# Kernel optimization log

Hardware: AMD Instinct MI355X
Metric: run time of the kernel (lower is better)

Reference implementation:

```python
import jax, jax.numpy as jnp
import numpy as np

B, N, D_IN, D_HID, D_OUT = 8, 512, 4608, 4608, 1152
DROP = 0.1
INV_SQRT2 = 0.7071067811865476
INV_SQRT_2PI = 0.3989422804014327


def _clean(s):
    # nan -> 1e-5, inf -> 1.0 (matches torch.where chain)
    return jnp.where(jnp.isnan(s), jnp.asarray(1e-5, s.dtype),
                     jnp.where(jnp.isinf(s), jnp.asarray(1.0, s.dtype), s))


def kl_regularizer(w_mu, w_sigma):
    d = w_mu.shape[0]
    ws = jax.nn.softplus(w_sigma)  # log(1+exp(w_sigma))
    return 0.5 * jnp.mean(d * ws + jnp.sum(w_mu * w_mu, axis=0) - d - d * jnp.log(ws))


def vdp_linear(mu_in, Sigma_in, w_mu, w_sigma):
    mu_out = jnp.matmul(mu_in, w_mu)                                 # [B,N,U]
    kl = kl_regularizer(w_mu, w_sigma)
    W_Sigma = jax.nn.softplus(w_sigma)                               # [U]
    Sigma_1 = jnp.matmul(Sigma_in, w_mu * w_mu)                      # w^T Sigma_in w (diag)
    Sigma_2 = jnp.sum(mu_in * mu_in, axis=-1, keepdims=True) * W_Sigma
    Sigma_3 = jnp.sum(Sigma_in, axis=-1, keepdims=True) * W_Sigma
    return mu_out, _clean(Sigma_1 + Sigma_2 + Sigma_3), kl


def vdp_gelu(mu_in, Sigma_in):
    # exact (erf) gelu and its analytic derivative: Phi(x) + x*phi(x)
    cdf = 0.5 * (1.0 + jax.lax.erf(mu_in * INV_SQRT2))
    pdf = jnp.exp(-0.5 * mu_in * mu_in) * INV_SQRT_2PI
    grad = cdf + mu_in * pdf
    return mu_in * cdf, grad * grad * Sigma_in


def vdp_dropout(mu_in, Sigma_in, mask):
    keep = 1.0 - DROP
    m = mask.astype(mu_in.dtype)
    mu_out = mu_in * m / keep                       # torch F.dropout scaling
    Sigma_out = Sigma_in * m / mu_in.shape[-1]      # kept Sigma values (unscaled), / units
    return mu_out, _clean(Sigma_out)


def setup_inputs() -> dict:
    key = jax.random.key(0)
    k = jax.random.split(key, 8)
    mu_in = jax.random.normal(k[0], (B, N, D_IN), dtype=jnp.float32)
    sigma_in = jax.random.uniform(k[1], (B, N, D_IN), dtype=jnp.float32)
    mask1 = jax.random.bernoulli(k[2], 1.0 - DROP, (B, N, D_HID))
    mask2 = jax.random.bernoulli(k[3], 1.0 - DROP, (B, N, D_OUT))
    w_mu1 = 0.05 * jax.random.normal(k[4], (D_IN, D_HID), dtype=jnp.float32)
    w_sigma1 = jnp.full((D_HID,), -4.6, dtype=jnp.float32)
    w_mu2 = 0.05 * jax.random.normal(k[5], (D_HID, D_OUT), dtype=jnp.float32)
    w_sigma2 = jnp.full((D_OUT,), -4.6, dtype=jnp.float32)
    return {"mu_in": mu_in, "sigma_in": sigma_in, "mask1": mask1, "mask2": mask2,
            "w_mu1": w_mu1, "w_sigma1": w_sigma1, "w_mu2": w_mu2, "w_sigma2": w_sigma2}


def reference(mu_in, sigma_in, mask1, mask2, w_mu1, w_sigma1, w_mu2, w_sigma2):
    mu, sig, kl1 = vdp_linear(mu_in, sigma_in, w_mu1, w_sigma1)
    mu, sig = vdp_gelu(mu, sig)
    mu, sig = vdp_dropout(mu, sig, mask1)
    mu, sig, kl2 = vdp_linear(mu, sig, w_mu2, w_sigma2)
    mu, sig = vdp_dropout(mu, sig, mask2)
    return mu, _clean(sig), kl1 + kl2
```

## Files before the change

kernel.cpp:

```cpp
#include <hip/hip_runtime.h>
#include <cstdint>
#include <cstddef>

static constexpr int Mrows = 4096;
static constexpr int K1 = 4608;
static constexpr int N1 = 4608;
static constexpr int N2 = 1152;
static constexpr int NPART1 = (K1 / 32) * (N1 / 32);
static constexpr int NPART2 = (K1 / 32) * (N2 / 32);

typedef float  f32x4  __attribute__((ext_vector_type(4)));
typedef __bf16 bf16x8 __attribute__((ext_vector_type(8)));

__device__ __forceinline__ unsigned short f2bf(float f) {
  unsigned int u = __float_as_uint(f);
  u += 0x7fffu + ((u >> 16) & 1u);
  return (unsigned short)(u >> 16);
}
__device__ __forceinline__ float bf2f(unsigned short h) {
  return __uint_as_float(((unsigned int)h) << 16);
}
__device__ __forceinline__ float cleanf(float s) {
  if (__builtin_isnan(s)) return 1e-5f;
  if (__builtin_isinf(s)) return 1.0f;
  return s;
}

__global__ __launch_bounds__(256) void prep_in(
    const float* __restrict__ mu, const float* __restrict__ sg,
    unsigned short* __restrict__ A1, unsigned short* __restrict__ As16,
    float* __restrict__ rmu2, float* __restrict__ rsg)
{
  const int row = blockIdx.x;
  const int tid = threadIdx.x;
  const float4* mup = (const float4*)(mu + (size_t)row * K1);
  const float4* sgp = (const float4*)(sg + (size_t)row * K1);
  ushort4* a1p = (ushort4*)(A1 + (size_t)row * K1);
  ushort4* asp = (ushort4*)(As16 + (size_t)row * K1);
  float smu = 0.f, ssg = 0.f;
  for (int j = tid; j < K1 / 4; j += 256) {
    float4 m4 = mup[j];
    float4 s4 = sgp[j];
    smu += m4.x*m4.x + m4.y*m4.y + m4.z*m4.z + m4.w*m4.w;
    ssg += s4.x + s4.y + s4.z + s4.w;
    a1p[j] = make_ushort4(f2bf(m4.x), f2bf(m4.y), f2bf(m4.z), f2bf(m4.w));
    asp[j] = make_ushort4(f2bf(s4.x), f2bf(s4.y), f2bf(s4.z), f2bf(s4.w));
  }
  __shared__ float red[2][4];
  for (int off = 32; off; off >>= 1) {
    smu += __shfl_down(smu, off);
    ssg += __shfl_down(ssg, off);
  }
  const int lane = tid & 63, wv = tid >> 6;
  if (!lane) { red[0][wv] = smu; red[1][wv] = ssg; }
  __syncthreads();
  if (tid == 0) {
    rmu2[row] = red[0][0] + red[0][1] + red[0][2] + red[0][3];
    rsg[row]  = red[1][0] + red[1][1] + red[1][2] + red[1][3];
  }
}

__global__ __launch_bounds__(256) void prep_w(
    const float* __restrict__ w, unsigned short* __restrict__ Bt,
    unsigned short* __restrict__ Bsq, float* __restrict__ partials,
    int K, int N)
{
  __shared__ float t[32][33];
  const int kt = blockIdx.x * 32;
  const int nt = blockIdx.y * 32;
  const int tx = threadIdx.x & 31;
  const int ty = threadIdx.x >> 5;
  float loc = 0.f;
#pragma unroll
  for (int i = 0; i < 32; i += 8) {
    float v = w[(size_t)(kt + ty + i) * N + (nt + tx)];
    t[ty + i][tx] = v;
    loc += v * v;
  }
  __syncthreads();
#pragma unroll
  for (int i = 0; i < 32; i += 8) {
    float v = t[tx][ty + i];
    size_t o = (size_t)(nt + ty + i) * K + (kt + tx);
    Bt[o]  = f2bf(v);
    Bsq[o] = f2bf(v * v);
  }
  __shared__ float red[4];
  for (int off = 32; off; off >>= 1) loc += __shfl_down(loc, off);
  const int lane = threadIdx.x & 63, wv = threadIdx.x >> 6;
  if (!lane) red[wv] = loc;
  __syncthreads();
  if (threadIdx.x == 0)
    partials[blockIdx.y * gridDim.x + blockIdx.x] = red[0] + red[1] + red[2] + red[3];
}

__global__ __launch_bounds__(256) void kl_prep(
    const float* __restrict__ wsig1, const float* __restrict__ wsig2,
    const float* __restrict__ part1, const float* __restrict__ part2,
    float* __restrict__ ws1, float* __restrict__ ws2, float* __restrict__ outkl)
{
  const int tid = threadIdx.x;
  float s1 = 0.f, l1 = 0.f, s2 = 0.f, l2 = 0.f, q1 = 0.f, q2 = 0.f;
  for (int j = tid; j < N1; j += 256) {
    float x = wsig1[j];
    float sp = (x > 20.f) ? x : log1pf(expf(x));
    ws1[j] = sp; s1 += sp; l1 += logf(sp);
  }
  for (int j = tid; j < N2; j += 256) {
    float x = wsig2[j];
    float sp = (x > 20.f) ? x : log1pf(expf(x));
    ws2[j] = sp; s2 += sp; l2 += logf(sp);
  }
  for (int j = tid; j < NPART1; j += 256) q1 += part1[j];
  for (int j = tid; j < NPART2; j += 256) q2 += part2[j];
  __shared__ float red[6][4];
  for (int off = 32; off; off >>= 1) {
    s1 += __shfl_down(s1, off); l1 += __shfl_down(l1, off);
    s2 += __shfl_down(s2, off); l2 += __shfl_down(l2, off);
    q1 += __shfl_down(q1, off); q2 += __shfl_down(q2, off);
  }
  const int lane = tid & 63, wv = tid >> 6;
  if (!lane) {
    red[0][wv] = s1; red[1][wv] = l1; red[2][wv] = s2;
    red[3][wv] = l2; red[4][wv] = q1; red[5][wv] = q2;
  }
  __syncthreads();
  if (tid == 0) {
    float S1v = red[0][0] + red[0][1] + red[0][2] + red[0][3];
    float L1v = red[1][0] + red[1][1] + red[1][2] + red[1][3];
    float S2v = red[2][0] + red[2][1] + red[2][2] + red[2][3];
    float L2v = red[3][0] + red[3][1] + red[3][2] + red[3][3];
    float Q1v = red[4][0] + red[4][1] + red[4][2] + red[4][3];
    float Q2v = red[5][0] + red[5][1] + red[5][2] + red[5][3];
    const float d = 4608.f;
    float kl1 = 0.5f * (d * (S1v / (float)N1) + Q1v / (float)N1 - d - d * (L1v / (float)N1));
    float kl2 = 0.5f * (d * (S2v / (float)N2) + Q2v / (float)N2 - d - d * (L2v / (float)N2));
    outkl[0] = kl1 + kl2;
  }
}

#define GLD16(gp, lp) __builtin_amdgcn_global_load_lds( \
    (__attribute__((address_space(1))) void*)(unsigned short*)(gp), \
    (__attribute__((address_space(3))) void*)(lp), 16, 0, 0)

__device__ __forceinline__ void storeC(float v, float* p) { *p = v; }
__device__ __forceinline__ void storeC(float v, unsigned short* p) { *p = f2bf(v); }

template <int NT, typename CT>
__global__ __launch_bounds__(512, 2) void gemm256(
    const unsigned short* __restrict__ Amu, const unsigned short* __restrict__ Asg,
    const unsigned short* __restrict__ Bmu, const unsigned short* __restrict__ Bsq,
    CT* __restrict__ Cmu, CT* __restrict__ Csg)
{
  __shared__ __align__(16) char smem[114688];
  char* lA = smem;
  char* lB = smem + 65536;

  const int tid  = threadIdx.x;
  const int lane = tid & 63;
  const int wave = tid >> 6;
  const int which = blockIdx.z;
  const unsigned short* Ag = which ? Asg : Amu;
  const unsigned short* Bg = which ? Bsq : Bmu;
  CT* Cg = which ? Csg : Cmu;

  const int m0 = blockIdx.y * 256;
  const int n0 = blockIdx.x * 192;
  const int wm = (wave >> 2) * 128;
  const int wn = (wave & 3) * 48;
  const int fm = lane & 15;
  const int kq = lane >> 4;

  const int rbase = tid >> 3;
  const int gg = (tid & 7) ^ (rbase & 7);
  const unsigned short* gA0 = Ag + (size_t)(m0 + rbase) * K1 + gg * 8;
  const unsigned short* gB0 = Bg + (size_t)(n0 + rbase) * K1 + gg * 8;

  auto stA = [&](int buf, int h, int kt2) {
    const unsigned short* g = gA0 + (size_t)h * 128 * K1 + (size_t)kt2 * 64;
    char* l = lA + buf * 32768 + h * 16384 + tid * 16;
    GLD16(g, l);
    GLD16(g + (size_t)64 * K1, l + 8192);
  };
  auto stB = [&](int buf, int kt2) {
    const unsigned short* g = gB0 + (size_t)kt2 * 64;
    char* l = lB + buf * 24576 + tid * 16;
    GLD16(g, l);
    GLD16(g + (size_t)64 * K1, l + 8192);
    GLD16(g + (size_t)128 * K1, l + 16384);
  };

  const int abase = (wm + fm) * 128;
  const int bbase = 65536 + (wn + fm) * 128;
  const int x0 = ((0 * 4 + kq) ^ (fm & 7)) * 16;
  const int x1 = ((1 * 4 + kq) ^ (fm & 7)) * 16;

  f32x4 acc[8][3];
#pragma unroll
  for (int i = 0; i < 8; ++i)
#pragma unroll
    for (int j = 0; j < 3; ++j) acc[i][j] = (f32x4){0.f, 0.f, 0.f, 0.f};

  stB(0, 0);
  stA(0, 0, 0); stA(0, 1, 0);
  stB(1, 1);
  asm volatile("s_waitcnt vmcnt(3)" ::: "memory");
  __builtin_amdgcn_s_barrier();

  const int ksteps = K1 / 64;
  for (int kt = 0; kt < ksteps; ++kt) {
    const int cur = kt & 1;
    const char* cA = lA + cur * 32768 + abase;
    const char* cB = smem + cur * 24576 + bbase;

    bf16x8 Af[8][2], Bf[3][2];

#pragma unroll
    for (int j = 0; j < 3; ++j) {
      Bf[j][0] = *(const bf16x8*)(cB + j * 2048 + x0);
      Bf[j][1] = *(const bf16x8*)(cB + j * 2048 + x1);
    }
#pragma unroll
    for (int i = 0; i < 4; ++i) {
      Af[i][0] = *(const bf16x8*)(cA + i * 2048 + x0);
      Af[i][1] = *(const bf16x8*)(cA + i * 2048 + x1);
    }
    if (kt + 1 < ksteps) stA(cur ^ 1, 0, kt + 1);
    asm volatile("s_waitcnt lgkmcnt(8)" ::: "memory");
    __builtin_amdgcn_s_barrier();
    asm volatile("s_waitcnt lgkmcnt(0)" ::: "memory");
    __builtin_amdgcn_s_setprio(1);
#pragma unroll
    for (int i = 0; i < 4; ++i)
#pragma unroll
      for (int j = 0; j < 2; ++j) {
        acc[i][j] = __builtin_amdgcn_mfma_f32_16x16x32_bf16(Af[i][0], Bf[j][0], acc[i][j], 0, 0, 0);
        acc[i][j] = __builtin_amdgcn_mfma_f32_16x16x32_bf16(Af[i][1], Bf[j][1], acc[i][j], 0, 0, 0);
      }
    __builtin_amdgcn_s_setprio(0);
    __builtin_amdgcn_s_barrier();

#pragma unroll
    for (int i = 4; i < 8; ++i) {
      Af[i][0] = *(const bf16x8*)(cA + i * 2048 + x0);
      Af[i][1] = *(const bf16x8*)(cA + i * 2048 + x1);
    }
    if (kt + 1 < ksteps) stA(cur ^ 1, 1, kt + 1);
    __builtin_amdgcn_s_barrier();
    asm volatile("s_waitcnt lgkmcnt(0)" ::: "memory");
    __builtin_amdgcn_s_setprio(1);
#pragma unroll
    for (int i = 4; i < 8; ++i)
#pragma unroll
      for (int j = 0; j < 2; ++j) {
        acc[i][j] = __builtin_amdgcn_mfma_f32_16x16x32_bf16(Af[i][0], Bf[j][0], acc[i][j], 0, 0, 0);
        acc[i][j] = __builtin_amdgcn_mfma_f32_16x16x32_bf16(Af[i][1], Bf[j][1], acc[i][j], 0, 0, 0);
      }
    __builtin_amdgcn_s_setprio(0);
    __builtin_amdgcn_s_barrier();

    if (kt + 2 < ksteps) stB(cur, kt + 2);
    __builtin_amdgcn_s_barrier();
    __builtin_amdgcn_s_setprio(1);
#pragma unroll
    for (int i = 0; i < 8; ++i) {
      acc[i][2] = __builtin_amdgcn_mfma_f32_16x16x32_bf16(Af[i][0], Bf[2][0], acc[i][2], 0, 0, 0);
      acc[i][2] = __builtin_amdgcn_mfma_f32_16x16x32_bf16(Af[i][1], Bf[2][1], acc[i][2], 0, 0, 0);
    }
    __builtin_amdgcn_s_setprio(0);
    if (kt < ksteps - 2) asm volatile("s_waitcnt vmcnt(3)" ::: "memory");
    else                 asm volatile("s_waitcnt vmcnt(0)" ::: "memory");
    __builtin_amdgcn_s_barrier();
  }

  const int rr = (lane >> 4) * 4;
  const int cc = lane & 15;
#pragma unroll
  for (int i = 0; i < 8; ++i) {
    const int grow = m0 + wm + i * 16 + rr;
#pragma unroll
    for (int j = 0; j < 3; ++j) {
      const int gcol = n0 + wn + j * 16 + cc;
      CT* cp = Cg + (size_t)grow * NT + gcol;
#pragma unroll
      for (int r = 0; r < 4; ++r) storeC(acc[i][j][r], cp + (size_t)r * NT);
    }
  }
}

__global__ __launch_bounds__(256) void mid_kernel(
    const unsigned short* __restrict__ mu1, const unsigned short* __restrict__ S1,
    const int* __restrict__ mask1, const float* __restrict__ ws1,
    const float* __restrict__ rmu2, const float* __restrict__ rsg,
    unsigned short* __restrict__ A2, unsigned short* __restrict__ As2,
    float* __restrict__ r2mu, float* __restrict__ r2sg)
{
  const int row = blockIdx.x;
  const int tid = threadIdx.x;
  const float rterm = rmu2[row] + rsg[row];
  const ushort4* mup = (const ushort4*)(mu1 + (size_t)row * N1);
  const ushort4* s1p = (const ushort4*)(S1 + (size_t)row * N1);
  const int4* mkp = (const int4*)(mask1 + (size_t)row * N1);
  const float4* wsp = (const float4*)ws1;
  ushort4* a2p = (ushort4*)(A2 + (size_t)row * N1);
  ushort4* as2p = (ushort4*)(As2 + (size_t)row * N1);
  float smu = 0.f, ssg = 0.f;
  for (int j = tid; j < N1 / 4; j += 256) {
    ushort4 m4 = mup[j]; ushort4 s4 = s1p[j]; int4 k4 = mkp[j]; float4 w4 = wsp[j];
    float xv[4] = {bf2f(m4.x), bf2f(m4.y), bf2f(m4.z), bf2f(m4.w)};
    float Sv[4] = {bf2f(s4.x), bf2f(s4.y), bf2f(s4.z), bf2f(s4.w)};
    float wv[4] = {w4.x, w4.y, w4.z, w4.w};
    int   kv[4] = {k4.x, k4.y, k4.z, k4.w};
    unsigned short oa[4], os[4];
#pragma unroll
    for (int t = 0; t < 4; t++) {
      float sig1 = cleanf(Sv[t] + rterm * wv[t]);
      float x = xv[t];
      float cdf = 0.5f * (1.f + erff(x * 0.70710678118654752f));
      float pdf = expf(-0.5f * x * x) * 0.3989422804014327f;
      float g = cdf + x * pdf;
      float mu2v = x * cdf;
      float sig2 = g * g * sig1;
      float mm = (float)kv[t];
      float mu3 = mu2v * mm * (1.f / 0.9f);
      float sig3 = cleanf(sig2 * mm * (1.f / 4608.f));
      smu += mu3 * mu3;
      ssg += sig3;
      oa[t] = f2bf(mu3);
      os[t] = f2bf(sig3);
    }
    a2p[j] = make_ushort4(oa[0], oa[1], oa[2], oa[3]);
    as2p[j] = make_ushort4(os[0], os[1], os[2], os[3]);
  }
  __shared__ float red[2][4];
  for (int off = 32; off; off >>= 1) {
    smu += __shfl_down(smu, off);
    ssg += __shfl_down(ssg, off);
  }
  const int lane = tid & 63, wv2 = tid >> 6;
  if (!lane) { red[0][wv2] = smu; red[1][wv2] = ssg; }
  __syncthreads();
  if (tid == 0) {
    r2mu[row] = red[0][0] + red[0][1] + red[0][2] + red[0][3];
    r2sg[row] = red[1][0] + red[1][1] + red[1][2] + red[1][3];
  }
}

__global__ __launch_bounds__(256) void final_kernel(
    const float* __restrict__ pmu, const float* __restrict__ psig,
    const int* __restrict__ mask2, const float* __restrict__ ws2,
    const float* __restrict__ r2mu, const float* __restrict__ r2sg,
    float* __restrict__ out_mu, float* __restrict__ out_sig)
{
  const int row = blockIdx.x;
  const int tid = threadIdx.x;
  const float rterm = r2mu[row] + r2sg[row];
  const float4* mup0 = (const float4*)(pmu + (size_t)row * N2);
  const float4* sbp0 = (const float4*)(psig + (size_t)row * N2);
  const int4* mkp = (const int4*)(mask2 + (size_t)row * N2);
  const float4* wsp = (const float4*)ws2;
  float4* omp = (float4*)(out_mu + (size_t)row * N2);
  float4* osp = (float4*)(out_sig + (size_t)row * N2);
  for (int j = tid; j < N2 / 4; j += 256) {
    float4 m4 = mup0[j];
    float4 sb = sbp0[j];
    int4 k4 = mkp[j]; float4 w4 = wsp[j];
    float mo[4], so[4];
    float mv[4] = {m4.x, m4.y, m4.z, m4.w};
    float sv[4] = {sb.x, sb.y, sb.z, sb.w};
    float wv[4] = {w4.x, w4.y, w4.z, w4.w};
    int   kv[4] = {k4.x, k4.y, k4.z, k4.w};
#pragma unroll
    for (int t = 0; t < 4; t++) {
      float sig4 = cleanf(sv[t] + rterm * wv[t]);
      float mm = (float)kv[t];
      float mu5 = mv[t] * mm * (1.f / 0.9f);
      float sig5 = cleanf(sig4 * mm * (1.f / 1152.f));
      mo[t] = mu5;
      so[t] = cleanf(sig5);
    }
    omp[j] = make_float4(mo[0], mo[1], mo[2], mo[3]);
    osp[j] = make_float4(so[0], so[1], so[2], so[3]);
  }
}

extern "C" void kernel_launch(void* const* d_in, const int* in_sizes, int n_in,
                              void* d_out, int out_size, void* d_ws, size_t ws_size,
                              hipStream_t stream)
{
  const float* mu_in = (const float*)d_in[0];
  const float* sg_in = (const float*)d_in[1];
  const int* mask1 = (const int*)d_in[2];
  const int* mask2 = (const int*)d_in[3];
  const float* w_mu1 = (const float*)d_in[4];
  const float* wsig1 = (const float*)d_in[5];
  const float* w_mu2 = (const float*)d_in[6];
  const float* wsig2 = (const float*)d_in[7];
  float* out = (float*)d_out;

  char* ws = (char*)d_ws;
  const size_t oA1  = 0;
  const size_t oAs  = oA1  + (size_t)37748736;
  const size_t oB1t = oAs  + (size_t)37748736;
  const size_t oB1q = oB1t + (size_t)42467328;
  const size_t oB2t = oB1q + (size_t)42467328;
  const size_t oB2q = oB2t + (size_t)10616832;
  const size_t oMu1 = oB2q + (size_t)10616832;
  const size_t oS1  = oMu1 + (size_t)37748736;
  const size_t oVec = oS1  + (size_t)37748736;

  unsigned short* A1     = (unsigned short*)(ws + oA1);
  unsigned short* As16   = (unsigned short*)(ws + oAs);
  unsigned short* B1t    = (unsigned short*)(ws + oB1t);
  unsigned short* B1sq16 = (unsigned short*)(ws + oB1q);
  unsigned short* B2t    = (unsigned short*)(ws + oB2t);
  unsigned short* B2sq16 = (unsigned short*)(ws + oB2q);
  unsigned short* mu1b   = (unsigned short*)(ws + oMu1);
  unsigned short* S1b16  = (unsigned short*)(ws + oS1);
  float* pmu  = (float*)(ws + oB1t);
  float* psig = (float*)(ws + oMu1);

  float* rmu2 = (float*)(ws + oVec);
  float* rsg  = rmu2 + Mrows;
  float* r2mu = rsg + Mrows;
  float* r2sg = r2mu + Mrows;
  float* ws1v = r2sg + Mrows;
  float* ws2v = ws1v + N1;
  float* part1 = ws2v + N2;
  float* part2 = part1 + NPART1;

  prep_in<<<Mrows, 256, 0, stream>>>(mu_in, sg_in, A1, As16, rmu2, rsg);
  prep_w<<<dim3(K1 / 32, N1 / 32), 256, 0, stream>>>(w_mu1, B1t, B1sq16, part1, K1, N1);
  prep_w<<<dim3(K1 / 32, N2 / 32), 256, 0, stream>>>(w_mu2, B2t, B2sq16, part2, K1, N2);
  kl_prep<<<1, 256, 0, stream>>>(wsig1, wsig2, part1, part2, ws1v, ws2v,
                                 out + (size_t)2 * Mrows * N2);

  gemm256<N1, unsigned short><<<dim3(N1 / 192, Mrows / 256, 2), 512, 0, stream>>>(
      A1, As16, B1t, B1sq16, mu1b, S1b16);

  mid_kernel<<<Mrows, 256, 0, stream>>>(mu1b, S1b16, mask1, ws1v, rmu2, rsg,
                                        A1, As16, r2mu, r2sg);

  gemm256<N2, float><<<dim3(N2 / 192, Mrows / 256, 2), 512, 0, stream>>>(
      A1, As16, B2t, B2sq16, pmu, psig);

  final_kernel<<<Mrows, 256, 0, stream>>>(pmu, psig, mask2, ws2v, r2mu, r2sg,
                                          out, out + (size_t)Mrows * N2);
  (void)in_sizes; (void)n_in; (void)out_size; (void)ws_size;
}
```

Before: 826.7 us.

## Fuse final dropout epilogue into second GEMM and merge weight prep kernels

Removes final_kernel by applying the mask2 dropout, sigma row/column terms and NaN/Inf cleaning directly in the second GEMM's epilogue, writing straight to the output. This avoids writing and re-reading the fp32 intermediate GEMM results. The two weight-transpose kernels are merged into one launch with 64x64 tiles, vectorized float4 loads and 8-wide bf16 stores. The fused epilogue reads mask values with scattered, less coalesced loads, and both the mu and sigma halves read the mask.

New measurement: 826.3 us. Within noise of the previous version (-0.0%).

```diff
diff --git a/kernel.cpp b/kernel.cpp
--- a/kernel.cpp
+++ b/kernel.cpp
@@ -6,11 +6,12 @@
 static constexpr int K1 = 4608;
 static constexpr int N1 = 4608;
 static constexpr int N2 = 1152;
-static constexpr int NPART1 = (K1 / 32) * (N1 / 32);
-static constexpr int NPART2 = (K1 / 32) * (N2 / 32);
+static constexpr int NPART1 = (K1 / 64) * (N1 / 64);
+static constexpr int NPART2 = (K1 / 64) * (N2 / 64);
 
 typedef float  f32x4  __attribute__((ext_vector_type(4)));
 typedef __bf16 bf16x8 __attribute__((ext_vector_type(8)));
+typedef unsigned short u16x8 __attribute__((ext_vector_type(8)));
 
 __device__ __forceinline__ unsigned short f2bf(float f) {
   unsigned int u = __float_as_uint(f);
@@ -60,38 +61,63 @@
   }
 }
 
-__global__ __launch_bounds__(256) void prep_w(
-    const float* __restrict__ w, unsigned short* __restrict__ Bt,
-    unsigned short* __restrict__ Bsq, float* __restrict__ partials,
-    int K, int N)
-{
-  __shared__ float t[32][33];
-  const int kt = blockIdx.x * 32;
-  const int nt = blockIdx.y * 32;
-  const int tx = threadIdx.x & 31;
-  const int ty = threadIdx.x >> 5;
+__global__ __launch_bounds__(256) void prep_w2x(
+    const float* __restrict__ w1, const float* __restrict__ w2,
+    unsigned short* __restrict__ B1t, unsigned short* __restrict__ B1sq,
+    unsigned short* __restrict__ B2t, unsigned short* __restrict__ B2sq,
+    float* __restrict__ part1, float* __restrict__ part2)
+{
+  const int ybl = blockIdx.y;
+  const bool is2 = ybl >= (N1 / 64);
+  const int nb = is2 ? (ybl - N1 / 64) : ybl;
+  const float* w = is2 ? w2 : w1;
+  unsigned short* Bt = is2 ? B2t : B1t;
+  unsigned short* Bq = is2 ? B2sq : B1sq;
+  float* parts = is2 ? part2 : part1;
+  const int N = is2 ? N2 : N1;
+
+  const int kt = blockIdx.x * 64;
+  const int nt = nb * 64;
+  const int tid = threadIdx.x;
+
+  __shared__ float t[64][65];
   float loc = 0.f;
-#pragma unroll
-  for (int i = 0; i < 32; i += 8) {
-    float v = w[(size_t)(kt + ty + i) * N + (nt + tx)];
-    t[ty + i][tx] = v;
-    loc += v * v;
+  {
+    const int r = tid >> 4;
+    const int c = (tid & 15) * 4;
+#pragma unroll
+    for (int p = 0; p < 4; ++p) {
+      const int k = p * 16 + r;
+      float4 v = *(const float4*)(w + (size_t)(kt + k) * N + nt + c);
+      t[k][c] = v.x; t[k][c + 1] = v.y; t[k][c + 2] = v.z; t[k][c + 3] = v.w;
+      loc += v.x*v.x + v.y*v.y + v.z*v.z + v.w*v.w;
+    }
   }
   __syncthreads();
-#pragma unroll
-  for (int i = 0; i < 32; i += 8) {
-    float v = t[tx][ty + i];
-    size_t o = (size_t)(nt + ty + i) * K + (kt + tx);
-    Bt[o]  = f2bf(v);
-    Bsq[o] = f2bf(v * v);
+  {
+    const int kk = (tid & 7) * 8;
+#pragma unroll
+    for (int q = 0; q < 2; ++q) {
+      const int n = (tid >> 3) + q * 32;
+      u16x8 bt, bq;
+#pragma unroll
+      for (int i = 0; i < 8; ++i) {
+        float v = t[kk + i][n];
+        bt[i] = f2bf(v);
+        bq[i] = f2bf(v * v);
+      }
+      size_t o = (size_t)(nt + n) * K1 + (kt + kk);
+      *(u16x8*)(Bt + o) = bt;
+      *(u16x8*)(Bq + o) = bq;
+    }
   }
   __shared__ float red[4];
   for (int off = 32; off; off >>= 1) loc += __shfl_down(loc, off);
-  const int lane = threadIdx.x & 63, wv = threadIdx.x >> 6;
+  const int lane = tid & 63, wv = tid >> 6;
   if (!lane) red[wv] = loc;
   __syncthreads();
-  if (threadIdx.x == 0)
-    partials[blockIdx.y * gridDim.x + blockIdx.x] = red[0] + red[1] + red[2] + red[3];
+  if (tid == 0)
+    parts[nb * (K1 / 64) + blockIdx.x] = red[0] + red[1] + red[2] + red[3];
 }
 
 __global__ __launch_bounds__(256) void kl_prep(
@@ -146,11 +172,13 @@
 __device__ __forceinline__ void storeC(float v, float* p) { *p = v; }
 __device__ __forceinline__ void storeC(float v, unsigned short* p) { *p = f2bf(v); }
 
-template <int NT, typename CT>
+template <int NT, typename CT, bool FUSE>
 __global__ __launch_bounds__(512, 2) void gemm256(
     const unsigned short* __restrict__ Amu, const unsigned short* __restrict__ Asg,
     const unsigned short* __restrict__ Bmu, const unsigned short* __restrict__ Bsq,
-    CT* __restrict__ Cmu, CT* __restrict__ Csg)
+    CT* __restrict__ Cmu, CT* __restrict__ Csg,
+    const int* __restrict__ mask2, const float* __restrict__ ws2,
+    const float* __restrict__ r2mu, const float* __restrict__ r2sg)
 {
   __shared__ __align__(16) char smem[114688];
   char* lA = smem;
@@ -275,15 +303,47 @@
 
   const int rr = (lane >> 4) * 4;
   const int cc = lane & 15;
-#pragma unroll
-  for (int i = 0; i < 8; ++i) {
-    const int grow = m0 + wm + i * 16 + rr;
-#pragma unroll
-    for (int j = 0; j < 3; ++j) {
-      const int gcol = n0 + wn + j * 16 + cc;
-      CT* cp = Cg + (size_t)grow * NT + gcol;
-#pragma unroll
-      for (int r = 0; r < 4; ++r) storeC(acc[i][j][r], cp + (size_t)r * NT);
+  if constexpr (!FUSE) {
+#pragma unroll
+    for (int i = 0; i < 8; ++i) {
+      const int grow = m0 + wm + i * 16 + rr;
+#pragma unroll
+      for (int j = 0; j < 3; ++j) {
+        const int gcol = n0 + wn + j * 16 + cc;
+        CT* cp = Cg + (size_t)grow * NT + gcol;
+#pragma unroll
+        for (int r = 0; r < 4; ++r) storeC(acc[i][j][r], cp + (size_t)r * NT);
+      }
+    }
+  } else {
+    const float inv_keep  = 1.f / 0.9f;
+    const float inv_units = 1.f / 1152.f;
+    float wcol[3];
+    if (which) {
+#pragma unroll
+      for (int j = 0; j < 3; ++j) wcol[j] = ws2[n0 + wn + j * 16 + cc];
+    }
+#pragma unroll
+    for (int i = 0; i < 8; ++i) {
+#pragma unroll
+      for (int r = 0; r < 4; ++r) {
+        const int grow = m0 + wm + i * 16 + rr + r;
+        const float rterm = which ? (r2mu[grow] + r2sg[grow]) : 0.f;
+#pragma unroll
+        for (int j = 0; j < 3; ++j) {
+          const int gcol = n0 + wn + j * 16 + cc;
+          const float mm = (float)mask2[(size_t)grow * NT + gcol];
+          const float v = acc[i][j][r];
+          float o;
+          if (which == 0) {
+            o = v * mm * inv_keep;
+          } else {
+            float sig4 = cleanf(v + rterm * wcol[j]);
+            o = cleanf(cleanf(sig4 * mm * inv_units));
+          }
+          Cg[(size_t)grow * NT + gcol] = (CT)o;
+        }
+      }
     }
   }
 }
@@ -346,44 +406,6 @@
   }
 }
 
-__global__ __launch_bounds__(256) void final_kernel(
-    const float* __restrict__ pmu, const float* __restrict__ psig,
-    const int* __restrict__ mask2, const float* __restrict__ ws2,
-    const float* __restrict__ r2mu, const float* __restrict__ r2sg,
-    float* __restrict__ out_mu, float* __restrict__ out_sig)
-{
-  const int row = blockIdx.x;
-  const int tid = threadIdx.x;
-  const float rterm = r2mu[row] + r2sg[row];
-  const float4* mup0 = (const float4*)(pmu + (size_t)row * N2);
-  const float4* sbp0 = (const float4*)(psig + (size_t)row * N2);
-  const int4* mkp = (const int4*)(mask2 + (size_t)row * N2);
-  const float4* wsp = (const float4*)ws2;
-  float4* omp = (float4*)(out_mu + (size_t)row * N2);
-  float4* osp = (float4*)(out_sig + (size_t)row * N2);
-  for (int j = tid; j < N2 / 4; j += 256) {
-    float4 m4 = mup0[j];
-    float4 sb = sbp0[j];
-    int4 k4 = mkp[j]; float4 w4 = wsp[j];
-    float mo[4], so[4];
-    float mv[4] = {m4.x, m4.y, m4.z, m4.w};
-    float sv[4] = {sb.x, sb.y, sb.z, sb.w};
-    float wv[4] = {w4.x, w4.y, w4.z, w4.w};
-    int   kv[4] = {k4.x, k4.y, k4.z, k4.w};
-#pragma unroll
-    for (int t = 0; t < 4; t++) {
-      float sig4 = cleanf(sv[t] + rterm * wv[t]);
-      float mm = (float)kv[t];
-      float mu5 = mv[t] * mm * (1.f / 0.9f);
-      float sig5 = cleanf(sig4 * mm * (1.f / 1152.f));
-      mo[t] = mu5;
-      so[t] = cleanf(sig5);
-    }
-    omp[j] = make_float4(mo[0], mo[1], mo[2], mo[3]);
-    osp[j] = make_float4(so[0], so[1], so[2], so[3]);
-  }
-}
-
 extern "C" void kernel_launch(void* const* d_in, const int* in_sizes, int n_in,
                               void* d_out, int out_size, void* d_ws, size_t ws_size,
                               hipStream_t stream)
@@ -417,8 +439,6 @@
   unsigned short* B2sq16 = (unsigned short*)(ws + oB2q);
   unsigned short* mu1b   = (unsigned short*)(ws + oMu1);
   unsigned short* S1b16  = (unsigned short*)(ws + oS1);
-  float* pmu  = (float*)(ws + oB1t);
-  float* psig = (float*)(ws + oMu1);
 
   float* rmu2 = (float*)(ws + oVec);
   float* rsg  = rmu2 + Mrows;
@@ -430,21 +450,20 @@
   float* part2 = part1 + NPART1;
 
   prep_in<<<Mrows, 256, 0, stream>>>(mu_in, sg_in, A1, As16, rmu2, rsg);
-  prep_w<<<dim3(K1 / 32, N1 / 32), 256, 0, stream>>>(w_mu1, B1t, B1sq16, part1, K1, N1);
-  prep_w<<<dim3(K1 / 32, N2 / 32), 256, 0, stream>>>(w_mu2, B2t, B2sq16, part2, K1, N2);
+  prep_w2x<<<dim3(K1 / 64, N1 / 64 + N2 / 64), 256, 0, stream>>>(
+      w_mu1, w_mu2, B1t, B1sq16, B2t, B2sq16, part1, part2);
   kl_prep<<<1, 256, 0, stream>>>(wsig1, wsig2, part1, part2, ws1v, ws2v,
                                  out + (size_t)2 * Mrows * N2);
 
-  gemm256<N1, unsigned short><<<dim3(N1 / 192, Mrows / 256, 2), 512, 0, stream>>>(
-      A1, As16, B1t, B1sq16, mu1b, S1b16);
+  gemm256<N1, unsigned short, false><<<dim3(N1 / 192, Mrows / 256, 2), 512, 0, stream>>>(
+      A1, As16, B1t, B1sq16, mu1b, S1b16, nullptr, nullptr, nullptr, nullptr);
 
   mid_kernel<<<Mrows, 256, 0, stream>>>(mu1b, S1b16, mask1, ws1v, rmu2, rsg,
                                         A1, As16, r2mu, r2sg);
 
-  gemm256<N2, float><<<dim3(N2 / 192, Mrows / 256, 2), 512, 0, stream>>>(
-      A1, As16, B2t, B2sq16, pmu, psig);
-
-  final_kernel<<<Mrows, 256, 0, stream>>>(pmu, psig, mask2, ws2v, r2mu, r2sg,
-                                          out, out + (size_t)Mrows * N2);
+  gemm256<N2, float, true><<<dim3(N2 / 192, Mrows / 256, 2), 512, 0, stream>>>(
+      A1, As16, B2t, B2sq16, out, out + (size_t)Mrows * N2,
+      mask2, ws2v, r2mu, r2sg);
+
   (void)in_sizes; (void)n_in; (void)out_size; (void)ws_size;
 }
```
